# Kernel tuning notes

Measured on AMD Instinct MI355X. Metric: run time of the kernel, lower is better.

Reference implementation:

```python
import jax, jax.numpy as jnp
import numpy as np

MAX_DEPTH = 8
LMBDA = 0.1
OUTPUT_DIM = 128


def setup_inputs() -> dict:
    key = jax.random.key(0)
    k1, k2, k3, k4, k5, k6 = jax.random.split(key, 6)
    B, D, C = 8192, 2048, OUTPUT_DIM
    n_inner = 2 ** MAX_DEPTH - 1  # 255 inner nodes, BFS order
    n_leaf = 2 ** MAX_DEPTH       # 256 leaves
    x = jax.random.normal(k1, (B, D), dtype=jnp.float32)
    target = jax.random.randint(k2, (B,), 0, C)
    # small scale so sigmoid gates are not saturated (log(pen), log(1-pen) finite)
    W = jax.random.normal(k3, (n_inner, D), dtype=jnp.float32) * 0.02
    b = jax.random.normal(k4, (n_inner,), dtype=jnp.float32) * 0.02
    beta = jax.random.normal(k5, (n_inner,), dtype=jnp.float32)
    leaf_params = jax.random.normal(k6, (n_leaf, C), dtype=jnp.float32)
    return {"x": x, "target": target, "W": W, "b": b, "beta": beta,
            "leaf_params": leaf_params}


def reference(x, target, W, b, beta, leaf_params):
    B = x.shape[0]
    C = leaf_params.shape[1]
    y = jax.nn.one_hot(target, C, dtype=x.dtype)  # target_onehot

    # All inner-node gates as one batched GEMM: p[b,i] = sigmoid(beta_i*(x@w_i+b_i))
    p = jax.nn.sigmoid(beta[None, :] * (x @ W.T + b[None, :]))  # [B, n_inner]

    # Level-by-level path probability propagation (BFS node order).
    path = jnp.ones((B, 1), x.dtype)
    penalties = []  # per-level [2^d] node penalties
    start = 0
    for d in range(MAX_DEPTH):
        n = 2 ** d
        p_lvl = p[:, start:start + n]                      # [B, 2^d]
        pen = jnp.sum(p_lvl * path, axis=0) / jnp.sum(path, axis=0)
        penalties.append(pen)
        # left child gets path*(1-p), right gets path*p; interleave -> next level
        path = jnp.stack([path * (1.0 - p_lvl), path * p_lvl], axis=-1).reshape(B, 2 * n)
        start += n
    # path: [B, n_leaf] leaf path probabilities (left-to-right order)

    Q = jax.nn.softmax(leaf_params, axis=-1)               # [n_leaf, C]
    TQ = y @ jnp.log(Q).T                                  # [B, n_leaf], y . log Q per leaf
    loss = jnp.mean(jnp.sum(path * TQ, axis=1))

    # Penalty C: only inner nodes whose children are NOT leaves contribute
    # (original get_penalty drops depth==max_depth nodes), depths 1..max_depth-1.
    Cpen = jnp.asarray(0.0, x.dtype)
    for d in range(MAX_DEPTH - 1):
        lam = LMBDA * 2.0 ** (-(d + 1))
        pen = penalties[d]
        Cpen = Cpen - lam * 0.5 * jnp.sum(jnp.log(pen) + jnp.log(1.0 - pen))

    total = -loss + Cpen

    # output: Q of the max-path-prob leaf per sample
    leaf_idx = jnp.argmax(path, axis=1)                    # [B]
    output = Q[leaf_idx]                                   # [B, C]
    return total, output
```

## Files before the change

kernel.cpp:

```cpp
#include <hip/hip_runtime.h>
#include <hip/hip_bf16.h>
#include <hip/hip_fp16.h>
#include <stdint.h>

#define B_SIZE 8192
#define D_SIZE 2048
#define C_SIZE 128
#define N_INNER 255
#define N_LEAF 256

#define GBM 32
#define BK 32
#define KHALF 1024
#define KITER (KHALF / BK)
#define NPADL 260

typedef _Float16 half8 __attribute__((ext_vector_type(8)));
typedef __fp16 pk16x2 __attribute__((ext_vector_type(2)));
typedef float f32x4 __attribute__((ext_vector_type(4)));

__device__ inline uint32_t pkh(float a, float b) {
    pk16x2 h = __builtin_amdgcn_cvt_pkrtz(a, b);
    return __builtin_bit_cast(uint32_t, h);
}
__device__ inline void split8(const float4 v0, const float4 v1, half8& hi, half8& lo) {
    pk16x2 a01 = __builtin_amdgcn_cvt_pkrtz(v0.x, v0.y);
    pk16x2 a23 = __builtin_amdgcn_cvt_pkrtz(v0.z, v0.w);
    pk16x2 a45 = __builtin_amdgcn_cvt_pkrtz(v1.x, v1.y);
    pk16x2 a67 = __builtin_amdgcn_cvt_pkrtz(v1.z, v1.w);
    uint4 h = make_uint4(__builtin_bit_cast(uint32_t, a01), __builtin_bit_cast(uint32_t, a23),
                         __builtin_bit_cast(uint32_t, a45), __builtin_bit_cast(uint32_t, a67));
    uint4 l = make_uint4(pkh(v0.x - (float)a01[0], v0.y - (float)a01[1]),
                         pkh(v0.z - (float)a23[0], v0.w - (float)a23[1]),
                         pkh(v1.x - (float)a45[0], v1.y - (float)a45[1]),
                         pkh(v1.z - (float)a67[0], v1.w - (float)a67[1]));
    hi = __builtin_bit_cast(half8, h);
    lo = __builtin_bit_cast(half8, l);
}

__global__ __launch_bounds__(128) void softmax_kernel(
    const float* __restrict__ lp, float* __restrict__ Q, float* __restrict__ logQt)
{
    int row = blockIdx.x;
    int t = threadIdx.x;
    __shared__ float red[128];
    float v = lp[row * C_SIZE + t];
    red[t] = v; __syncthreads();
    for (int s = 64; s > 0; s >>= 1) { if (t < s) red[t] = fmaxf(red[t], red[t + s]); __syncthreads(); }
    float mx = red[0]; __syncthreads();
    float e = expf(v - mx);
    red[t] = e; __syncthreads();
    for (int s = 64; s > 0; s >>= 1) { if (t < s) red[t] += red[t + s]; __syncthreads(); }
    float sum = red[0];
    Q[row * C_SIZE + t] = e / sum;
    logQt[(size_t)t * N_LEAF + row] = (v - mx) - logf(sum);
}

__global__ __launch_bounds__(512, 2) void fused_kernel(
    const float* __restrict__ x, const float* __restrict__ W,
    const float* __restrict__ bvec, const float* __restrict__ beta,
    const float* __restrict__ Q, const float* __restrict__ logQt,
    const int* __restrict__ target,
    float* __restrict__ g_num, float* __restrict__ g_den, float* __restrict__ g_loss,
    float* __restrict__ out)
{
    __shared__ __align__(16) float zbuf[2][GBM][NPADL];
    __shared__ float s_num[128], s_den[128], s_loss;

    const int t = threadIdx.x;
    const int lane = t & 63, w = t >> 6;
    const int kg = w >> 2, nw = w & 3;
    const int lr = lane & 15, lq = lane >> 4;
    const int m0 = blockIdx.x * GBM;
    const int kb0 = kg * KHALF;

    if (t < 128) s_num[t] = 0.f;
    else if (t < 256) s_den[t - 128] = 0.f;
    if (t == 0) s_loss = 0.f;

    f32x4 acc[2][4];
    #pragma unroll
    for (int mt = 0; mt < 2; ++mt)
        #pragma unroll
        for (int nt = 0; nt < 4; ++nt) acc[mt][nt] = (f32x4){0.f, 0.f, 0.f, 0.f};

    float4 aA[4], bA[8], aB[4], bB[8];

    #define LOAD_A(dst, kb)                                                            \
        _Pragma("unroll")                                                              \
        for (int mt = 0; mt < 2; ++mt) {                                               \
            const float* base = x + (size_t)(m0 + mt * 16 + lr) * D_SIZE + (kb) + lq * 8; \
            dst[mt * 2 + 0] = *(const float4*)base;                                    \
            dst[mt * 2 + 1] = *(const float4*)(base + 4);                              \
        }
    #define LOAD_B(dst, kb)                                                            \
        _Pragma("unroll")                                                              \
        for (int nt = 0; nt < 4; ++nt) {                                               \
            int row = nw * 64 + nt * 16 + lr;                                          \
            bool ok = row < N_INNER;                                                   \
            const float* base = W + (size_t)(ok ? row : 0) * D_SIZE + (kb) + lq * 8;   \
            float4 v0 = *(const float4*)base;                                          \
            float4 v1 = *(const float4*)(base + 4);                                    \
            if (!ok) { v0 = make_float4(0.f,0.f,0.f,0.f); v1 = v0; }                   \
            dst[nt * 2 + 0] = v0; dst[nt * 2 + 1] = v1;                                \
        }
    #define GEMM_STEP(cur_a, cur_b, nxt_a, nxt_b, kbn)                                 \
        {                                                                              \
            LOAD_A(nxt_a, kbn); LOAD_B(nxt_b, kbn);                                    \
            half8 ah[2], al[2], bh[4], bl[4];                                          \
            _Pragma("unroll")                                                          \
            for (int mt = 0; mt < 2; ++mt) split8(cur_a[mt*2], cur_a[mt*2+1], ah[mt], al[mt]); \
            _Pragma("unroll")                                                          \
            for (int nt = 0; nt < 4; ++nt) split8(cur_b[nt*2], cur_b[nt*2+1], bh[nt], bl[nt]); \
            _Pragma("unroll")                                                          \
            for (int mt = 0; mt < 2; ++mt)                                             \
                _Pragma("unroll")                                                      \
                for (int nt = 0; nt < 4; ++nt) {                                       \
                    acc[mt][nt] = __builtin_amdgcn_mfma_f32_16x16x32_f16(ah[mt], bh[nt], acc[mt][nt], 0, 0, 0); \
                    acc[mt][nt] = __builtin_amdgcn_mfma_f32_16x16x32_f16(ah[mt], bl[nt], acc[mt][nt], 0, 0, 0); \
                    acc[mt][nt] = __builtin_amdgcn_mfma_f32_16x16x32_f16(al[mt], bh[nt], acc[mt][nt], 0, 0, 0); \
                }                                                                      \
        }

    LOAD_A(aA, kb0); LOAD_B(bA, kb0);
    int kb = kb0;
    #pragma unroll 1
    for (int kt = 0; kt < KITER; kt += 2) {
        int kb1 = kb + BK;
        int kb2 = (kt + 2 < KITER) ? kb + 2 * BK : kb;
        GEMM_STEP(aA, bA, aB, bB, kb1);
        GEMM_STEP(aB, bB, aA, bA, kb2);
        kb += 2 * BK;
    }

    #pragma unroll
    for (int mt = 0; mt < 2; ++mt)
        #pragma unroll
        for (int nt = 0; nt < 4; ++nt)
            #pragma unroll
            for (int r = 0; r < 4; ++r)
                zbuf[kg][mt * 16 + lq * 4 + r][nw * 64 + nt * 16 + lr] = acc[mt][nt][r];
    __syncthreads();

    const int c0 = lane * 4;
    float bet[4], bia[4];
    #pragma unroll
    for (int j = 0; j < 4; ++j) {
        int c = c0 + j;
        bet[j] = (c < N_INNER) ? beta[c] : 0.f;
        bia[j] = (c < N_INNER) ? bvec[c] : 0.f;
    }
    float pnum[4] = {0.f, 0.f, 0.f, 0.f};
    float pden[4] = {0.f, 0.f, 0.f, 0.f};
    float loss = 0.f;

    for (int i = 0; i < 4; ++i) {
        int rl = w * 4 + i;
        int r = m0 + rl;
        float4 za = *(const float4*)&zbuf[0][rl][c0];
        float4 zb = *(const float4*)&zbuf[1][rl][c0];
        float zv[4] = {za.x + zb.x, za.y + zb.y, za.z + zb.z, za.w + zb.w};
        float pv[4];
        #pragma unroll
        for (int j = 0; j < 4; ++j) {
            int c = c0 + j;
            pv[j] = (c < N_INNER) ? 1.f / (1.f + expf(-bet[j] * (zv[j] + bia[j]))) : 0.f;
        }
        *(float4*)&zbuf[0][rl][c0] = make_float4(pv[0], pv[1], pv[2], pv[3]);
        asm volatile("s_waitcnt lgkmcnt(0)" ::: "memory");

        int tg = target[r];
        float4 lq4 = *(const float4*)(logQt + (size_t)tg * N_LEAF + c0);
        float lqa[4] = {lq4.x, lq4.y, lq4.z, lq4.w};
        float lsum = 0.f, bestV = -1.f;
        int bestI = 0;
        #pragma unroll
        for (int j = 0; j < 4; ++j) {
            int leaf = c0 + j;
            float pl = 1.f;
            #pragma unroll
            for (int d = 0; d < 8; ++d) {
                int node = (1 << d) - 1 + (leaf >> (8 - d));
                int bit = (leaf >> (7 - d)) & 1;
                float pvn = zbuf[0][rl][node];
                pl *= bit ? pvn : (1.f - pvn);
            }
            lsum += pl * lqa[j];
            if (pl > bestV) { bestV = pl; bestI = leaf; }
        }
        if (lane < 32) {
            #pragma unroll
            for (int j = 0; j < 4; ++j) {
                int c = c0 + j;
                if (c < 127) {
                    int h = c + 1; int d = 31 - __clz(h);
                    float pp = 1.f;
                    for (int e = 0; e < d; ++e) {
                        int ha = h >> (d - e);
                        int bit = (h >> (d - 1 - e)) & 1;
                        float pvn = zbuf[0][rl][ha - 1];
                        pp *= bit ? pvn : (1.f - pvn);
                    }
                    pnum[j] += zbuf[0][rl][c] * pp;
                    pden[j] += pp;
                }
            }
        }
        #pragma unroll
        for (int m = 1; m < 64; m <<= 1) {
            lsum += __shfl_xor(lsum, m, 64);
            float ov = __shfl_xor(bestV, m, 64);
            int   oi = __shfl_xor(bestI, m, 64);
            if (ov > bestV || (ov == bestV && oi < bestI)) { bestV = ov; bestI = oi; }
        }
        loss += lsum;
        out[1 + (size_t)r * C_SIZE + lane]      = Q[bestI * C_SIZE + lane];
        out[1 + (size_t)r * C_SIZE + lane + 64] = Q[bestI * C_SIZE + lane + 64];
    }

    if (lane < 32) {
        #pragma unroll
        for (int j = 0; j < 4; ++j) {
            int c = c0 + j;
            if (c < 127) {
                atomicAdd(&s_num[c], pnum[j]);
                atomicAdd(&s_den[c], pden[j]);
            }
        }
    }
    if (lane == 0) atomicAdd(&s_loss, loss);
    __syncthreads();
    if (t < 127)                    atomicAdd(&g_num[t], s_num[t]);
    else if (t >= 128 && t < 255)   atomicAdd(&g_den[t - 128], s_den[t - 128]);
    else if (t == 256)              atomicAdd(g_loss, s_loss);
}

__global__ __launch_bounds__(128) void finalize_kernel(
    const float* __restrict__ g_num, const float* __restrict__ g_den,
    const float* __restrict__ g_loss, float* __restrict__ out)
{
    __shared__ float red[128];
    int t = threadIdx.x;
    float term = 0.f;
    if (t < 127) {
        int d = 31 - __clz(t + 1);
        float lam = 0.1f * exp2f(-(float)(d + 1));
        float pen = g_num[t] / g_den[t];
        term = lam * 0.5f * (logf(pen) + logf(1.f - pen));
    }
    red[t] = term; __syncthreads();
    for (int s = 64; s > 0; s >>= 1) { if (t < s) red[t] += red[t + s]; __syncthreads(); }
    if (t == 0) out[0] = -(g_loss[0] / (float)B_SIZE) - red[0];
}

extern "C" void kernel_launch(void* const* d_in, const int* in_sizes, int n_in,
                              void* d_out, int out_size, void* d_ws, size_t ws_size,
                              hipStream_t stream)
{
    const float* x    = (const float*)d_in[0];
    const int*   tgt  = (const int*)d_in[1];
    const float* W    = (const float*)d_in[2];
    const float* b    = (const float*)d_in[3];
    const float* beta = (const float*)d_in[4];
    const float* lp   = (const float*)d_in[5];
    float* out = (float*)d_out;

    float* g_acc = (float*)d_ws;
    float* Q     = g_acc + 512;
    float* logQt = Q + (size_t)N_LEAF * C_SIZE;

    (void)hipMemsetAsync(d_ws, 0, 512 * sizeof(float), stream);

    softmax_kernel<<<N_LEAF, 128, 0, stream>>>(lp, Q, logQt);

    fused_kernel<<<B_SIZE / GBM, 512, 0, stream>>>(
        x, W, b, beta, Q, logQt, tgt,
        g_acc, g_acc + 128, g_acc + 256, out);

    finalize_kernel<<<1, 128, 0, stream>>>(g_acc, g_acc + 128, g_acc + 256, out);
}
```

Measured before the change: 207.0 us.

## Pre-split W to fp16 hi/lo and stage split x tiles in LDS

A prep kernel now splits W into fp16 high and low parts once per call, alongside the leaf softmax. The main GEMM stages x through LDS, where it is split once and shared by all waves, instead of every wave loading and splitting fp32 A and B in registers. The block grows to 1024 threads across four K-groups, and their partial sums are combined with LDS atomicAdd into one z buffer. This removes repeated fp32-to-fp16 split work and halves W traffic, at the cost of two extra barriers per K step, LDS atomics, and heavy register pressure from launch_bounds(1024,4).

Result: slower. 225.9 us (+9.1%).

```diff
diff --git a/kernel.cpp b/kernel.cpp
--- a/kernel.cpp
+++ b/kernel.cpp
@@ -10,61 +10,84 @@
 #define N_LEAF 256
 
 #define GBM 32
-#define BK 32
-#define KHALF 1024
-#define KITER (KHALF / BK)
+#define BKW 32
+#define NKG 4
+#define KITER 16
+#define LDA 136
 #define NPADL 260
 
 typedef _Float16 half8 __attribute__((ext_vector_type(8)));
 typedef __fp16 pk16x2 __attribute__((ext_vector_type(2)));
 typedef float f32x4 __attribute__((ext_vector_type(4)));
+typedef unsigned short u16;
 
 __device__ inline uint32_t pkh(float a, float b) {
     pk16x2 h = __builtin_amdgcn_cvt_pkrtz(a, b);
     return __builtin_bit_cast(uint32_t, h);
 }
-__device__ inline void split8(const float4 v0, const float4 v1, half8& hi, half8& lo) {
-    pk16x2 a01 = __builtin_amdgcn_cvt_pkrtz(v0.x, v0.y);
-    pk16x2 a23 = __builtin_amdgcn_cvt_pkrtz(v0.z, v0.w);
-    pk16x2 a45 = __builtin_amdgcn_cvt_pkrtz(v1.x, v1.y);
-    pk16x2 a67 = __builtin_amdgcn_cvt_pkrtz(v1.z, v1.w);
-    uint4 h = make_uint4(__builtin_bit_cast(uint32_t, a01), __builtin_bit_cast(uint32_t, a23),
-                         __builtin_bit_cast(uint32_t, a45), __builtin_bit_cast(uint32_t, a67));
-    uint4 l = make_uint4(pkh(v0.x - (float)a01[0], v0.y - (float)a01[1]),
-                         pkh(v0.z - (float)a23[0], v0.w - (float)a23[1]),
-                         pkh(v1.x - (float)a45[0], v1.y - (float)a45[1]),
-                         pkh(v1.z - (float)a67[0], v1.w - (float)a67[1]));
-    hi = __builtin_bit_cast(half8, h);
-    lo = __builtin_bit_cast(half8, l);
-}
-
-__global__ __launch_bounds__(128) void softmax_kernel(
+__device__ inline void split4(const float4 v, uint2& hi, uint2& lo) {
+    pk16x2 a01 = __builtin_amdgcn_cvt_pkrtz(v.x, v.y);
+    pk16x2 a23 = __builtin_amdgcn_cvt_pkrtz(v.z, v.w);
+    float r0 = v.x - (float)a01[0];
+    float r1 = v.y - (float)a01[1];
+    float r2 = v.z - (float)a23[0];
+    float r3 = v.w - (float)a23[1];
+    hi = make_uint2(__builtin_bit_cast(uint32_t, a01), __builtin_bit_cast(uint32_t, a23));
+    lo = make_uint2(pkh(r0, r1), pkh(r2, r3));
+}
+
+__global__ __launch_bounds__(256) void prep_kernel(
+    const float* __restrict__ Wsrc, u16* __restrict__ Wh, u16* __restrict__ Wl,
     const float* __restrict__ lp, float* __restrict__ Q, float* __restrict__ logQt)
 {
-    int row = blockIdx.x;
+    int bid = blockIdx.x;
     int t = threadIdx.x;
-    __shared__ float red[128];
-    float v = lp[row * C_SIZE + t];
-    red[t] = v; __syncthreads();
-    for (int s = 64; s > 0; s >>= 1) { if (t < s) red[t] = fmaxf(red[t], red[t + s]); __syncthreads(); }
-    float mx = red[0]; __syncthreads();
-    float e = expf(v - mx);
-    red[t] = e; __syncthreads();
-    for (int s = 64; s > 0; s >>= 1) { if (t < s) red[t] += red[t + s]; __syncthreads(); }
-    float sum = red[0];
-    Q[row * C_SIZE + t] = e / sum;
-    logQt[(size_t)t * N_LEAF + row] = (v - mx) - logf(sum);
-}
-
-__global__ __launch_bounds__(512, 2) void fused_kernel(
-    const float* __restrict__ x, const float* __restrict__ W,
+    if (bid < 256) {
+        int row = bid;
+        int k = t * 8;
+        uint2 h0, l0, h1, l1;
+        if (row < N_INNER) {
+            float4 v0 = *(const float4*)(Wsrc + (size_t)row * D_SIZE + k);
+            float4 v1 = *(const float4*)(Wsrc + (size_t)row * D_SIZE + k + 4);
+            split4(v0, h0, l0); split4(v1, h1, l1);
+        } else {
+            h0 = l0 = h1 = l1 = make_uint2(0u, 0u);
+        }
+        *(uint2*)&Wh[(size_t)row * D_SIZE + k]     = h0;
+        *(uint2*)&Wh[(size_t)row * D_SIZE + k + 4] = h1;
+        *(uint2*)&Wl[(size_t)row * D_SIZE + k]     = l0;
+        *(uint2*)&Wl[(size_t)row * D_SIZE + k + 4] = l1;
+    } else {
+        int row = bid - 256;
+        __shared__ float red[128];
+        float v = 0.f;
+        if (t < 128) { v = lp[row * C_SIZE + t]; red[t] = v; }
+        __syncthreads();
+        for (int s = 64; s > 0; s >>= 1) { if (t < s) red[t] = fmaxf(red[t], red[t + s]); __syncthreads(); }
+        float mx = red[0]; __syncthreads();
+        float e = 0.f;
+        if (t < 128) { e = expf(v - mx); red[t] = e; }
+        __syncthreads();
+        for (int s = 64; s > 0; s >>= 1) { if (t < s) red[t] += red[t + s]; __syncthreads(); }
+        float sum = red[0];
+        if (t < 128) {
+            Q[row * C_SIZE + t] = e / sum;
+            logQt[(size_t)t * N_LEAF + row] = (v - mx) - logf(sum);
+        }
+    }
+}
+
+__global__ __launch_bounds__(1024, 4) void fused_kernel(
+    const float* __restrict__ x, const u16* __restrict__ Wh, const u16* __restrict__ Wl,
     const float* __restrict__ bvec, const float* __restrict__ beta,
     const float* __restrict__ Q, const float* __restrict__ logQt,
     const int* __restrict__ target,
     float* __restrict__ g_num, float* __restrict__ g_den, float* __restrict__ g_loss,
     float* __restrict__ out)
 {
-    __shared__ __align__(16) float zbuf[2][GBM][NPADL];
+    __shared__ __align__(16) u16 sAh[GBM * LDA];
+    __shared__ __align__(16) u16 sAl[GBM * LDA];
+    __shared__ __align__(16) float zbuf[GBM][NPADL];
     __shared__ float s_num[128], s_den[128], s_loss;
 
     const int t = threadIdx.x;
@@ -72,8 +95,8 @@
     const int kg = w >> 2, nw = w & 3;
     const int lr = lane & 15, lq = lane >> 4;
     const int m0 = blockIdx.x * GBM;
-    const int kb0 = kg * KHALF;
-
+
+    for (int i = t; i < GBM * NPADL; i += 1024) ((float*)zbuf)[i] = 0.f;
     if (t < 128) s_num[t] = 0.f;
     else if (t < 256) s_den[t - 128] = 0.f;
     if (t == 0) s_loss = 0.f;
@@ -84,53 +107,47 @@
         #pragma unroll
         for (int nt = 0; nt < 4; ++nt) acc[mt][nt] = (f32x4){0.f, 0.f, 0.f, 0.f};
 
-    float4 aA[4], bA[8], aB[4], bB[8];
-
-    #define LOAD_A(dst, kb)                                                            \
-        _Pragma("unroll")                                                              \
-        for (int mt = 0; mt < 2; ++mt) {                                               \
-            const float* base = x + (size_t)(m0 + mt * 16 + lr) * D_SIZE + (kb) + lq * 8; \
-            dst[mt * 2 + 0] = *(const float4*)base;                                    \
-            dst[mt * 2 + 1] = *(const float4*)(base + 4);                              \
-        }
-    #define LOAD_B(dst, kb)                                                            \
-        _Pragma("unroll")                                                              \
-        for (int nt = 0; nt < 4; ++nt) {                                               \
-            int row = nw * 64 + nt * 16 + lr;                                          \
-            bool ok = row < N_INNER;                                                   \
-            const float* base = W + (size_t)(ok ? row : 0) * D_SIZE + (kb) + lq * 8;   \
-            float4 v0 = *(const float4*)base;                                          \
-            float4 v1 = *(const float4*)(base + 4);                                    \
-            if (!ok) { v0 = make_float4(0.f,0.f,0.f,0.f); v1 = v0; }                   \
-            dst[nt * 2 + 0] = v0; dst[nt * 2 + 1] = v1;                                \
-        }
-    #define GEMM_STEP(cur_a, cur_b, nxt_a, nxt_b, kbn)                                 \
-        {                                                                              \
-            LOAD_A(nxt_a, kbn); LOAD_B(nxt_b, kbn);                                    \
-            half8 ah[2], al[2], bh[4], bl[4];                                          \
-            _Pragma("unroll")                                                          \
-            for (int mt = 0; mt < 2; ++mt) split8(cur_a[mt*2], cur_a[mt*2+1], ah[mt], al[mt]); \
-            _Pragma("unroll")                                                          \
-            for (int nt = 0; nt < 4; ++nt) split8(cur_b[nt*2], cur_b[nt*2+1], bh[nt], bl[nt]); \
-            _Pragma("unroll")                                                          \
-            for (int mt = 0; mt < 2; ++mt)                                             \
-                _Pragma("unroll")                                                      \
-                for (int nt = 0; nt < 4; ++nt) {                                       \
-                    acc[mt][nt] = __builtin_amdgcn_mfma_f32_16x16x32_f16(ah[mt], bh[nt], acc[mt][nt], 0, 0, 0); \
-                    acc[mt][nt] = __builtin_amdgcn_mfma_f32_16x16x32_f16(ah[mt], bl[nt], acc[mt][nt], 0, 0, 0); \
-                    acc[mt][nt] = __builtin_amdgcn_mfma_f32_16x16x32_f16(al[mt], bh[nt], acc[mt][nt], 0, 0, 0); \
-                }                                                                      \
-        }
-
-    LOAD_A(aA, kb0); LOAD_B(bA, kb0);
-    int kb = kb0;
+    const int srow = t >> 5;
+    const int sk   = (t & 31) * 4;
+    const int skg  = sk >> 5;
+    const int sko  = sk & 31;
+    const float* aptr = x + (size_t)(m0 + srow) * D_SIZE + skg * 512 + sko;
+
+    float4 av = *(const float4*)aptr;
+
     #pragma unroll 1
-    for (int kt = 0; kt < KITER; kt += 2) {
-        int kb1 = kb + BK;
-        int kb2 = (kt + 2 < KITER) ? kb + 2 * BK : kb;
-        GEMM_STEP(aA, bA, aB, bB, kb1);
-        GEMM_STEP(aB, bB, aA, bA, kb2);
-        kb += 2 * BK;
+    for (int kt = 0; kt < KITER; ++kt) {
+        __syncthreads();
+        {
+            uint2 hi, lo; split4(av, hi, lo);
+            *(uint2*)&sAh[srow * LDA + sk] = hi;
+            *(uint2*)&sAl[srow * LDA + sk] = lo;
+        }
+        __syncthreads();
+        if (kt + 1 < KITER) av = *(const float4*)(aptr + (kt + 1) * BKW);
+        const int kbB = kg * 512 + kt * BKW;
+        half8 bh[4], bl[4];
+        #pragma unroll
+        for (int nt = 0; nt < 4; ++nt) {
+            int row = nw * 64 + nt * 16 + lr;
+            bh[nt] = *(const half8*)(Wh + (size_t)row * D_SIZE + kbB + lq * 8);
+            bl[nt] = *(const half8*)(Wl + (size_t)row * D_SIZE + kbB + lq * 8);
+        }
+        half8 ah[2], al[2];
+        #pragma unroll
+        for (int mt = 0; mt < 2; ++mt) {
+            int off = (mt * 16 + lr) * LDA + kg * 32 + lq * 8;
+            ah[mt] = *(const half8*)&sAh[off];
+            al[mt] = *(const half8*)&sAl[off];
+        }
+        #pragma unroll
+        for (int mt = 0; mt < 2; ++mt)
+            #pragma unroll
+            for (int nt = 0; nt < 4; ++nt) {
+                acc[mt][nt] = __builtin_amdgcn_mfma_f32_16x16x32_f16(ah[mt], bh[nt], acc[mt][nt], 0, 0, 0);
+                acc[mt][nt] = __builtin_amdgcn_mfma_f32_16x16x32_f16(ah[mt], bl[nt], acc[mt][nt], 0, 0, 0);
+                acc[mt][nt] = __builtin_amdgcn_mfma_f32_16x16x32_f16(al[mt], bh[nt], acc[mt][nt], 0, 0, 0);
+            }
     }
 
     #pragma unroll
@@ -139,7 +156,7 @@
         for (int nt = 0; nt < 4; ++nt)
             #pragma unroll
             for (int r = 0; r < 4; ++r)
-                zbuf[kg][mt * 16 + lq * 4 + r][nw * 64 + nt * 16 + lr] = acc[mt][nt][r];
+                atomicAdd(&zbuf[mt * 16 + lq * 4 + r][nw * 64 + nt * 16 + lr], acc[mt][nt][r]);
     __syncthreads();
 
     const int c0 = lane * 4;
@@ -154,19 +171,18 @@
     float pden[4] = {0.f, 0.f, 0.f, 0.f};
     float loss = 0.f;
 
-    for (int i = 0; i < 4; ++i) {
-        int rl = w * 4 + i;
+    for (int i = 0; i < 2; ++i) {
+        int rl = w * 2 + i;
         int r = m0 + rl;
-        float4 za = *(const float4*)&zbuf[0][rl][c0];
-        float4 zb = *(const float4*)&zbuf[1][rl][c0];
-        float zv[4] = {za.x + zb.x, za.y + zb.y, za.z + zb.z, za.w + zb.w};
+        float4 zv4 = *(const float4*)&zbuf[rl][c0];
+        float zv[4] = {zv4.x, zv4.y, zv4.z, zv4.w};
         float pv[4];
         #pragma unroll
         for (int j = 0; j < 4; ++j) {
             int c = c0 + j;
             pv[j] = (c < N_INNER) ? 1.f / (1.f + expf(-bet[j] * (zv[j] + bia[j]))) : 0.f;
         }
-        *(float4*)&zbuf[0][rl][c0] = make_float4(pv[0], pv[1], pv[2], pv[3]);
+        *(float4*)&zbuf[rl][c0] = make_float4(pv[0], pv[1], pv[2], pv[3]);
         asm volatile("s_waitcnt lgkmcnt(0)" ::: "memory");
 
         int tg = target[r];
@@ -182,7 +198,7 @@
             for (int d = 0; d < 8; ++d) {
                 int node = (1 << d) - 1 + (leaf >> (8 - d));
                 int bit = (leaf >> (7 - d)) & 1;
-                float pvn = zbuf[0][rl][node];
+                float pvn = zbuf[rl][node];
                 pl *= bit ? pvn : (1.f - pvn);
             }
             lsum += pl * lqa[j];
@@ -198,10 +214,10 @@
                     for (int e = 0; e < d; ++e) {
                         int ha = h >> (d - e);
                         int bit = (h >> (d - 1 - e)) & 1;
-                        float pvn = zbuf[0][rl][ha - 1];
+                        float pvn = zbuf[rl][ha - 1];
                         pp *= bit ? pvn : (1.f - pvn);
                     }
-                    pnum[j] += zbuf[0][rl][c] * pp;
+                    pnum[j] += zbuf[rl][c] * pp;
                     pden[j] += pp;
                 }
             }
@@ -268,13 +284,15 @@
     float* g_acc = (float*)d_ws;
     float* Q     = g_acc + 512;
     float* logQt = Q + (size_t)N_LEAF * C_SIZE;
+    u16*   Wh    = (u16*)(logQt + (size_t)C_SIZE * N_LEAF);
+    u16*   Wl    = Wh + (size_t)N_LEAF * D_SIZE;
 
     (void)hipMemsetAsync(d_ws, 0, 512 * sizeof(float), stream);
 
-    softmax_kernel<<<N_LEAF, 128, 0, stream>>>(lp, Q, logQt);
-
-    fused_kernel<<<B_SIZE / GBM, 512, 0, stream>>>(
-        x, W, b, beta, Q, logQt, tgt,
+    prep_kernel<<<512, 256, 0, stream>>>(W, Wh, Wl, lp, Q, logQt);
+
+    fused_kernel<<<B_SIZE / GBM, 1024, 0, stream>>>(
+        x, Wh, Wl, b, beta, Q, logQt, tgt,
         g_acc, g_acc + 128, g_acc + 256, out);
 
     finalize_kernel<<<1, 128, 0, stream>>>(g_acc, g_acc + 128, g_acc + 256, out);
```
